# Kernel optimization log

Measured on AMD Instinct MI355X. Metric: run time of the kernel, lower is better.

## Reference

```python
import jax, jax.numpy as jnp
import numpy as np

DIM = 512
NUM_GROUPS = 32
EPS = 1e-6
INV_SQRT2 = 0.7071067811865476


def group_norm(x, gamma, beta):
    # x: [b, c, h, w]; GroupNorm with NUM_GROUPS groups, per-channel affine
    b, c, h, w = x.shape
    xg = x.reshape(b, NUM_GROUPS, c // NUM_GROUPS, h, w)
    mu = xg.mean(axis=(2, 3, 4), keepdims=True)
    var = xg.var(axis=(2, 3, 4), keepdims=True)
    xn = ((xg - mu) * jax.lax.rsqrt(var + EPS)).reshape(b, c, h, w)
    return xn * gamma[None, :, None, None] + beta[None, :, None, None]


def conv1x1(x, w, b):
    # 1x1 conv == per-pixel GEMM over channels. w: [out_c, in_c], b: [out_c]
    return jnp.einsum('oc,bchw->bohw', w, x) + b[None, :, None, None]


def setup_inputs() -> dict:
    key = jax.random.key(0)
    ks = jax.random.split(key, 6)
    b, c, h, w = 4, DIM, 64, 64
    q = jax.random.normal(ks[0], (b, c, h, w), dtype=jnp.float32)
    init = lambda k: jax.random.normal(k, (DIM, DIM), dtype=jnp.float32) * 0.02
    return {
        'q': q,
        'gamma': jnp.ones((DIM,), jnp.float32),
        'beta': jnp.zeros((DIM,), jnp.float32),
        'wq': init(ks[1]), 'bq': jnp.zeros((DIM,), jnp.float32),
        'wk': init(ks[2]), 'bk': jnp.zeros((DIM,), jnp.float32),
        'wv': init(ks[3]), 'bv': jnp.zeros((DIM,), jnp.float32),
        'wo': init(ks[4]), 'bo': jnp.zeros((DIM,), jnp.float32),
    }


def reference(q, gamma, beta, wq, bq, wk, bk, wv, bv, wo, bo):
    q_in = q
    x = group_norm(q, gamma, beta)  # self-attention path: v is None -> v = normed q
    qp = conv1x1(x, wq, bq)
    kp = conv1x1(x, wk, bk)
    vp = conv1x1(x, wv, bv)
    b, c, h, w = qp.shape
    qf = qp.reshape(b, c, h * w)
    kf = kp.reshape(b, c, h * w)
    vf = vp.reshape(b, c, h * w)
    # scores[b, i, j] = sum_c k[b,c,i] * q[b,c,j]; softmax over i (key axis, dim=-2)
    scores = jnp.einsum('bci,bcj->bij', kf, qf) * (c ** -0.5)
    attn = jax.nn.softmax(scores, axis=-2)
    out = jnp.einsum('bci,bij->bcj', vf, attn).reshape(b, c, h, w)
    out = conv1x1(out, wo, bo)
    return (out + q_in) * INV_SQRT2
```

## Files before the change

### kernel.cpp

```cpp
#include <hip/hip_runtime.h>

typedef __bf16 bf16;
typedef __bf16 bf16x4 __attribute__((ext_vector_type(4)));
typedef __bf16 bf16x8 __attribute__((ext_vector_type(8)));
typedef float floatx4 __attribute__((ext_vector_type(4)));
typedef float floatx16 __attribute__((ext_vector_type(16)));

#define SCALE_QK 0.044194173824159216f
#define INV_SQRT2F 0.7071067811865476f
#define TEN  8388608L
#define SBAT 2097152L

typedef const __attribute__((address_space(1))) void GV;
typedef __attribute__((address_space(3))) void SV;

__global__ __launch_bounds__(256) void detect_k(
    const unsigned* __restrict__ q, int* __restrict__ flag)
{
    __shared__ int cnt;
    if (threadIdx.x == 0) cnt = 0;
    __syncthreads();
    int c = 0;
    for (int i = threadIdx.x; i < 4096; i += 256) {
        unsigned e = (q[i] >> 7) & 0xFFu;
        c += (e >= 100u && e <= 140u) ? 1 : 0;
    }
    atomicAdd(&cnt, c);
    __syncthreads();
    if (threadIdx.x == 0) *flag = (cnt < 3000) ? 1 : 0;
}

__global__ __launch_bounds__(256) void convw_k(
    const void* w0, const void* w1, const void* w2, const void* w3,
    bf16* __restrict__ dst, const int* __restrict__ flag)
{
    const void* srcs[4] = {w0, w1, w2, w3};
    const void* s = srcs[blockIdx.y];
    bf16* d = dst + (size_t)blockIdx.y * 262144;
    const int i = (blockIdx.x * 256 + threadIdx.x) * 8;
    bf16x8 v;
    if (*flag) {
        const float* f = (const float*)s;
        #pragma unroll
        for (int r = 0; r < 8; ++r) v[r] = (bf16)f[i + r];
    } else {
        v = *(const bf16x8*)((const bf16*)s + i);
    }
    *(bf16x8*)(d + i) = v;
}

__global__ __launch_bounds__(256) void convp_k(
    const void* p0, const void* p1, const void* p2,
    const void* p3, const void* p4, const void* p5,
    float* __restrict__ dst, const int* __restrict__ flag)
{
    const void* srcs[6] = {p0, p1, p2, p3, p4, p5};
    const int f = *flag;
    for (int i = threadIdx.x; i < 3072; i += 256) {
        const void* s = srcs[i >> 9];
        const int off = i & 511;
        dst[i] = f ? ((const float*)s)[off] : (float)((const bf16*)s)[off];
    }
}

__global__ __launch_bounds__(256) void groupnorm_k(
    const void* __restrict__ qraw, const float* __restrict__ gamma,
    const float* __restrict__ beta, bf16* __restrict__ XN,
    const int* __restrict__ flag)
{
    const int tid = threadIdx.x;
    const int b = blockIdx.x >> 5, g = blockIdx.x & 31;
    const int f32 = *flag;
    const size_t base = ((size_t)b * 512 + (size_t)g * 16) * 4096;
    const float* sf = (const float*)qraw + base;
    const bf16*  sb = (const bf16*)qraw + base;

    float sum = 0.f, sq = 0.f;
    if (f32) {
        const floatx4* v4 = (const floatx4*)sf;
        for (int idx = tid; idx < 16384; idx += 256) {
            floatx4 v = v4[idx];
            #pragma unroll
            for (int r = 0; r < 4; ++r) { float f = v[r]; sum += f; sq += f * f; }
        }
    } else {
        const bf16x8* v8 = (const bf16x8*)sb;
        for (int idx = tid; idx < 8192; idx += 256) {
            bf16x8 v = v8[idx];
            #pragma unroll
            for (int r = 0; r < 8; ++r) { float f = (float)v[r]; sum += f; sq += f * f; }
        }
    }
    #pragma unroll
    for (int off = 32; off; off >>= 1) {
        sum += __shfl_down(sum, off);
        sq  += __shfl_down(sq, off);
    }
    __shared__ float sS[4], sQ[4];
    __shared__ float s_mean, s_rstd;
    const int wave = tid >> 6, lane = tid & 63;
    if (lane == 0) { sS[wave] = sum; sQ[wave] = sq; }
    __syncthreads();
    if (tid == 0) {
        float ts = sS[0] + sS[1] + sS[2] + sS[3];
        float tq = sQ[0] + sQ[1] + sQ[2] + sQ[3];
        float mean = ts * (1.0f / 65536.0f);
        float var  = tq * (1.0f / 65536.0f) - mean * mean;
        s_mean = mean;
        s_rstd = rsqrtf(fmaxf(var, 0.f) + 1e-6f);
    }
    __syncthreads();
    const float mean = s_mean, rstd = s_rstd;

    float ga[16], be[16];
    #pragma unroll
    for (int c = 0; c < 16; ++c) {
        ga[c] = gamma[g * 16 + c] * rstd;
        be[c] = beta[g * 16 + c] - mean * ga[c];
    }
    bf16* dst = XN + (size_t)b * SBAT + (size_t)g * 16;
    for (int p0 = 0; p0 < 4096; p0 += 256) {
        const int p = p0 + tid;
        bf16x8 o0, o1;
        #pragma unroll
        for (int c = 0; c < 8; ++c) {
            float v = f32 ? sf[(size_t)c * 4096 + p] : (float)sb[(size_t)c * 4096 + p];
            o0[c] = (bf16)(v * ga[c] + be[c]);
        }
        #pragma unroll
        for (int c = 0; c < 8; ++c) {
            float v = f32 ? sf[(size_t)(c + 8) * 4096 + p] : (float)sb[(size_t)(c + 8) * 4096 + p];
            o1[c] = (bf16)(v * ga[c + 8] + be[c + 8]);
        }
        bf16* dp = dst + (size_t)p * 512;
        *(bf16x8*)dp = o0;
        *(bf16x8*)(dp + 8) = o1;
    }
}

__global__ __launch_bounds__(512, 1) void fused_attn(
    const bf16* __restrict__ QKt,
    const bf16* __restrict__ V,
    bf16* __restrict__ AOt)
{
    __shared__ __align__(16) char smc[147456];

    const int tid = threadIdx.x;
    const int w = tid >> 6, lane = tid & 63;
    const int fr = lane & 15, quad = lane >> 4;
    const int l5 = lane >> 5, l31 = lane & 31;

    const int ll = blockIdx.x;
    const int xcd = ll & 7, rr = ll >> 3;
    const int b = xcd >> 1;
    const int j0 = ((xcd & 1) * 32 + rr) * 64;

    const bf16* Qb = QKt + (size_t)b * 4194304;
    const bf16* Kb = Qb + 512;
    const bf16* Vb = V + (size_t)b * SBAT;

    const int jb = w >> 1;
    const int kb = w & 1;
    const int wmP = (w >> 2) * 32;
    const int wnP = (w & 3) * 128;

    bf16x8 qf[16];
    {
        const bf16* qsrc = Qb + (size_t)(j0 + jb * 16 + fr) * 1024 + quad * 8;
        #pragma unroll
        for (int s = 0; s < 16; ++s) qf[s] = *(const bf16x8*)(qsrc + s * 32);
    }

    const int lcK = ((tid & 15) ^ ((tid >> 4) & 7)) << 3;
    const int rowK = tid >> 4;
    auto stageK = [&](int key0, int kd0, int buf) {
        char* d = smc + buf * 32768;
        const bf16* s0 = Kb + (size_t)(key0 + rowK) * 1024 + kd0 + lcK;
        #pragma unroll
        for (int rho = 0; rho < 4; ++rho)
            __builtin_amdgcn_global_load_lds((GV*)(s0 + (size_t)rho * 32 * 1024),
                (SV*)(d + rho * 8192 + tid * 16), 16, 0, 0);
    };
    const int lcV = ((tid & 3) ^ ((tid >> 3) & 3)) << 3;
    const int rowV = tid >> 2;
    auto stageV = [&](int i0, int buf) {
        char* d = smc + 65536 + buf * 32768;
        const bf16* s0 = Vb + (size_t)rowV * 4096 + i0 + lcV;
        #pragma unroll
        for (int rho = 0; rho < 4; ++rho)
            __builtin_amdgcn_global_load_lds((GV*)(s0 + (size_t)rho * 128 * 4096),
                (SV*)(d + rho * 8192 + tid * 16), 16, 0, 0);
    };

    const int kxor = fr & 7;
    const int kaddr0 = (kb * 64 + fr) * 256;
    const int prow_ = jb * 16 + fr;
    const int pxor = (prow_ & 7) << 4;
    char* const pbase = smc + 131072 + prow_ * 256;

    const int prowR = wmP + l31;
    const int swzP = (prowR & 7) << 4;

    floatx16 acc_o[4] = {};
    float l_acc = 0.f;

    stageK(0, 0, 0);

    for (int c = 0; c < 32; ++c) {
        const int k0 = c * 128;
        floatx4 acc_s[4] = {};

        #pragma unroll
        for (int s = 0; s < 4; ++s) {
            asm volatile("s_waitcnt vmcnt(0)" ::: "memory");
            __builtin_amdgcn_s_barrier();
            if (s < 3) stageK(k0, (s + 1) * 128, (s + 1) & 1);
            else       stageV(k0, 0);
            const char* kbuf = smc + (s & 1) * 32768;
            __builtin_amdgcn_s_setprio(1);
            #pragma unroll
            for (int ksl = 0; ksl < 4; ++ksl) {
                #pragma unroll
                for (int kf = 0; kf < 4; ++kf) {
                    bf16x8 kf8 = *(const bf16x8*)(kbuf + kaddr0 + kf * 4096 +
                        ((((ksl << 2) | quad) ^ kxor) << 4));
                    acc_s[kf] = __builtin_amdgcn_mfma_f32_16x16x32_bf16(
                        kf8, qf[s * 4 + ksl], acc_s[kf], 0, 0, 0);
                }
            }
            __builtin_amdgcn_s_setprio(0);
        }

        {
            float rs = 0.f;
            #pragma unroll
            for (int kf = 0; kf < 4; ++kf) {
                bf16x4 pk;
                #pragma unroll
                for (int r = 0; r < 4; ++r) {
                    float e = __expf(fminf(acc_s[kf][r] * SCALE_QK, 30.f));
                    rs += e;
                    pk[r] = (bf16)e;
                }
                *(bf16x4*)(pbase + ((kb * 128 + kf * 32 + quad * 8) ^ pxor)) = pk;
            }
            rs += __shfl_xor(rs, 16);
            rs += __shfl_xor(rs, 32);
            l_acc += rs;
            asm volatile("s_waitcnt lgkmcnt(0)" ::: "memory");
        }

        #pragma unroll
        for (int sv = 0; sv < 4; ++sv) {
            asm volatile("s_waitcnt vmcnt(0)" ::: "memory");
            __builtin_amdgcn_s_barrier();
            if (sv < 3)          stageV(k0 + (sv + 1) * 32, (sv + 1) & 1);
            else if (c < 31)     stageK(k0 + 128, 0, 0);
            const char* vb = smc + 65536 + (sv & 1) * 32768;
            const char* pb = smc + 131072;
            __builtin_amdgcn_s_setprio(1);
            #pragma unroll
            for (int ih = 0; ih < 2; ++ih) {
                const int is = sv * 2 + ih;
                bf16x8 pa = *(const bf16x8*)(pb + prowR * 256 +
                    ((is * 32 + l5 * 16) ^ swzP));
                #pragma unroll
                for (int nf = 0; nf < 4; ++nf) {
                    const int cc = wnP + nf * 32 + l31;
                    bf16x8 vb8 = *(const bf16x8*)(vb + cc * 64 +
                        ((ih * 32 + l5 * 16) ^ (((cc >> 1) & 3) << 4)));
                    acc_o[nf] = __builtin_amdgcn_mfma_f32_32x32x16_bf16(
                        pa, vb8, acc_o[nf], 0, 0, 0);
                }
            }
            __builtin_amdgcn_s_setprio(0);
        }
    }
    asm volatile("s_waitcnt vmcnt(0)" ::: "memory");
    __syncthreads();

    float* lsh = (float*)smc;
    if (lane < 16) lsh[w * 16 + lane] = l_acc;
    __syncthreads();
    float* rsh = (float*)(smc + 512);
    if (tid < 64) {
        const int jbq = tid >> 4, t = tid & 15;
        rsh[tid] = 1.0f / fmaxf(lsh[jbq * 32 + t] + lsh[jbq * 32 + 16 + t], 1e-30f);
    }
    __syncthreads();

    bf16* out = AOt + (size_t)b * SBAT + (size_t)j0 * 512;
    #pragma unroll
    for (int reg = 0; reg < 16; ++reg) {
        const int j = wmP + (reg & 3) + 8 * (reg >> 2) + 4 * l5;
        const float rl = rsh[j];
        #pragma unroll
        for (int nf = 0; nf < 4; ++nf) {
            const int cc = wnP + nf * 32 + l31;
            out[(size_t)j * 512 + cc] = (bf16)(acc_o[nf][reg] * rl);
        }
    }
}

template <int EPI>
__global__ __launch_bounds__(256, 4) void gemm_xyt(
    const bf16* __restrict__ Xb, const bf16* __restrict__ Yb,
    void* __restrict__ Cv, int N, int K, int lda, int ldb,
    long sX, long sY, long sC,
    const float* __restrict__ bias,
    const void* __restrict__ res, long sR,
    const int* __restrict__ flag)
{
    __shared__ __align__(16) bf16 smem[17408];

    const int tid  = threadIdx.x;
    const int wave = tid >> 6;
    const int lane = tid & 63;
    const int z = blockIdx.z;

    int bx = blockIdx.x, by = blockIdx.y;
    {
        const int gx = gridDim.x, gy = gridDim.y;
        const int o = by * gx + bx;
        const int xcd = o & 7, idx = o >> 3;
        if (gx == 8) {
            bx = xcd;
            by = idx;
        } else if (gx == 32 && gy == 4) {
            bx = (xcd & 1) * 16 + (idx & 15);
            by = xcd >> 1;
        }
    }

    const bf16* X = Xb + (long)z * sX;
    const bf16* Y = Yb + (long)z * sY;
    bf16*  Cb = (bf16*)Cv  + (long)z * sC;
    float* Cf = (float*)Cv + (long)z * sC;
    const int f32o = (EPI == 4) ? *flag : 0;

    const int m0 = by * 128, n0 = bx * 128;
    const int wm = (wave >> 1) * 64, wn = (wave & 1) * 64;
    const int fr = lane & 15, quad = lane >> 4;

    const int srow = tid >> 2;
    const int scol = (tid & 3) * 8;
    const bf16* pX = X + (size_t)(m0 + srow) * lda + scol;
    const bf16* pY = Y + (size_t)(n0 + srow) * ldb + scol;
    const size_t oX = (size_t)64 * lda, oY = (size_t)64 * ldb;
    char* const sb0 = (char*)smem;
    const int ldst = tid * 16;

    auto stage = [&](int k, int pb) {
        char* d = sb0 + pb * 16384;
        const bf16* x = pX + k * 32;
        const bf16* y = pY + k * 32;
        __builtin_amdgcn_global_load_lds((GV*)x,        (SV*)(d + ldst),         16, 0, 0);
        __builtin_amdgcn_global_load_lds((GV*)(x + oX), (SV*)(d + 4096 + ldst),  16, 0, 0);
        __builtin_amdgcn_global_load_lds((GV*)y,        (SV*)(d + 8192 + ldst),  16, 0, 0);
        __builtin_amdgcn_global_load_lds((GV*)(y + oY), (SV*)(d + 12288 + ldst), 16, 0, 0);
    };

    floatx4 acc[4][4] = {};
    const int NK = K >> 5;

    stage(0, 0);
    __syncthreads();

    for (int k = 0; k < NK; ++k) {
        const int p = k & 1;
        if (k + 1 < NK) stage(k + 1, 1 - p);
        const bf16* bA = smem + p * 8192;
        const bf16* bB = bA + 4096;
        bf16x8 af[4], bfr[4];
        #pragma unroll
        for (int i = 0; i < 4; ++i) {
            af[i]  = *(const bf16x8*)&bA[(wm + i * 16 + fr) * 32 + quad * 8];
            bfr[i] = *(const bf16x8*)&bB[(wn + i * 16 + fr) * 32 + quad * 8];
        }
        #pragma unroll
        for (int i = 0; i < 4; ++i)
            #pragma unroll
            for (int j = 0; j < 4; ++j)
                acc[i][j] = __builtin_amdgcn_mfma_f32_16x16x32_bf16(
                    af[i], bfr[j], acc[i][j], 0, 0, 0);
        __syncthreads();
    }

    #pragma unroll
    for (int i = 0; i < 4; ++i) {
        const int mg = m0 + wm + i * 16 + quad * 4;
        float bmr[4];
        if (EPI == 1 || EPI == 4) {
            #pragma unroll
            for (int r = 0; r < 4; ++r) bmr[r] = bias[mg + r];
        }
        #pragma unroll
        for (int j = 0; j < 4; ++j) {
            const int ng = n0 + wn + j * 16 + fr;
            #pragma unroll
            for (int r = 0; r < 4; ++r) {
                float v = acc[i][j][r];
                if (EPI == 0) v += bias[ng];
                if (EPI == 1) v += bmr[r];
                if (EPI == 4) v += bmr[r];
                acc[i][j][r] = v;
            }
        }
    }

    if (EPI != 4) {
        bf16* ct = smem;
        #pragma unroll
        for (int i = 0; i < 4; ++i)
            #pragma unroll
            for (int j = 0; j < 4; ++j)
                #pragma unroll
                for (int r = 0; r < 4; ++r)
                    ct[(wm + i * 16 + quad * 4 + r) * 132 + wn + j * 16 + fr] =
                        (bf16)acc[i][j][r];
        __syncthreads();
        #pragma unroll
        for (int w = 0; w < 8; ++w) {
            const int idx = w * 2048 + tid * 8;
            const int row = idx >> 7, col = idx & 127;
            bf16x8 v = *(const bf16x8*)&ct[row * 132 + col];
            *(bf16x8*)&Cb[(size_t)(m0 + row) * N + n0 + col] = v;
        }
    } else if (f32o) {
        float* ct = (float*)smem;
        const float* rres = (const float*)res + (size_t)z * sR;
        #pragma unroll
        for (int h = 0; h < 2; ++h) {
            if ((wave >> 1) == h) {
                #pragma unroll
                for (int i = 0; i < 4; ++i)
                    #pragma unroll
                    for (int j = 0; j < 4; ++j)
                        #pragma unroll
                        for (int r = 0; r < 4; ++r)
                            ct[(i * 16 + quad * 4 + r) * 132 + wn + j * 16 + fr] =
                                acc[i][j][r];
            }
            __syncthreads();
            #pragma unroll
            for (int w = 0; w < 8; ++w) {
                const int idx = (w * 256 + tid) * 4;
                const int row = idx >> 7, col = idx & 127;
                const size_t o = (size_t)(m0 + h * 64 + row) * N + n0 + col;
                floatx4 v = *(const floatx4*)&ct[row * 132 + col];
                floatx4 rv = *(const floatx4*)&rres[o];
                #pragma unroll
                for (int e = 0; e < 4; ++e) v[e] = (v[e] + rv[e]) * INV_SQRT2F;
                *(floatx4*)&Cf[o] = v;
            }
            __syncthreads();
        }
    } else {
        const bf16* resb = (const bf16*)res + (size_t)z * sR;
        #pragma unroll
        for (int i = 0; i < 4; ++i) {
            const int mg = m0 + wm + i * 16 + quad * 4;
            #pragma unroll
            for (int j = 0; j < 4; ++j) {
                const int ng = n0 + wn + j * 16 + fr;
                #pragma unroll
                for (int r = 0; r < 4; ++r) {
                    const size_t o = (size_t)(mg + r) * N + ng;
                    Cb[o] = (bf16)((acc[i][j][r] + (float)resb[o]) * INV_SQRT2F);
                }
            }
        }
    }
}

extern "C" void kernel_launch(void* const* d_in, const int* in_sizes, int n_in,
                              void* d_out, int out_size, void* d_ws, size_t ws_size,
                              hipStream_t stream)
{
    const void* q     = d_in[0];
    const void* gamma = d_in[1];
    const void* beta  = d_in[2];
    const void* wq    = d_in[3];
    const void* bq    = d_in[4];
    const void* wk    = d_in[5];
    const void* bk    = d_in[6];
    const void* wv    = d_in[7];
    const void* bv    = d_in[8];
    const void* wo    = d_in[9];
    const void* bo    = d_in[10];

    char* w = (char*)d_ws;
    int*   flag = (int*)w;   w += 16;
    float* Pf   = (float*)w; w += 6 * 512 * 4;
    bf16*  Wc   = (bf16*)w;  w += 4 * 262144 * 2;
    bf16*  XN   = (bf16*)w;  w += TEN * 2;
    bf16*  QKt  = (bf16*)w;  w += (size_t)4 * 4096 * 1024 * 2;
    bf16*  V    = (bf16*)w;  w += TEN * 2;
    bf16*  AOt  = XN;

    detect_k<<<dim3(1), 256, 0, stream>>>((const unsigned*)q, flag);
    convw_k<<<dim3(128, 4), 256, 0, stream>>>(wq, wk, wv, wo, Wc, flag);
    convp_k<<<dim3(1), 256, 0, stream>>>(gamma, beta, bq, bk, bv, bo, Pf, flag);

    groupnorm_k<<<dim3(128), 256, 0, stream>>>(q, Pf, Pf + 512, XN, flag);

    gemm_xyt<0><<<dim3(8, 32, 4), 256, 0, stream>>>(XN, Wc, QKt,
        1024, 512, 512, 512, SBAT, 0, (long)4096 * 1024, Pf + 1024,
        nullptr, 0, flag);
    gemm_xyt<1><<<dim3(32, 4, 4), 256, 0, stream>>>(Wc + 2 * 262144, XN, V,
        4096, 512, 512, 512, 0, SBAT, SBAT, Pf + 2048,
        nullptr, 0, flag);

    fused_attn<<<dim3(256), 512, 0, stream>>>(QKt, V, AOt);

    gemm_xyt<4><<<dim3(32, 4, 4), 256, 0, stream>>>(Wc + 3 * 262144, AOt, d_out,
        4096, 512, 512, 512, 0, SBAT, SBAT, Pf + 2560,
        q, SBAT, flag);
}
```

Measured before the change: 473.4 us.

## Warp-specialize attention kernel: QK/softmax waves and PV waves run software-pipelined

Splits the 8 waves of the attention block into two roles. Four waves compute QK^T scores and the exp for each 128-key chunk, while the other four compute the P·V accumulation for the previous chunk. Each stage now issues both the K and V loads, so the QK and PV phases of consecutive chunks overlap instead of running back to back. The cost is per-wave register pressure (8 score accumulators, or 2x4 32x32 accumulators), one extra pipeline iteration, and added barriers. The K swizzle widens to 16 rows, and the P buffer is now single-buffered while being shared across chunks.

```diff
diff --git a/kernel.cpp b/kernel.cpp
--- a/kernel.cpp
+++ b/kernel.cpp
@@ -159,19 +159,7 @@
     const bf16* Kb = Qb + 512;
     const bf16* Vb = V + (size_t)b * SBAT;
 
-    const int jb = w >> 1;
-    const int kb = w & 1;
-    const int wmP = (w >> 2) * 32;
-    const int wnP = (w & 3) * 128;
-
-    bf16x8 qf[16];
-    {
-        const bf16* qsrc = Qb + (size_t)(j0 + jb * 16 + fr) * 1024 + quad * 8;
-        #pragma unroll
-        for (int s = 0; s < 16; ++s) qf[s] = *(const bf16x8*)(qsrc + s * 32);
-    }
-
-    const int lcK = ((tid & 15) ^ ((tid >> 4) & 7)) << 3;
+    const int lcK = ((tid & 15) ^ ((tid >> 4) & 15)) << 3;
     const int rowK = tid >> 4;
     auto stageK = [&](int key0, int kd0, int buf) {
         char* d = smc + buf * 32768;
@@ -191,113 +179,139 @@
             __builtin_amdgcn_global_load_lds((GV*)(s0 + (size_t)rho * 128 * 4096),
                 (SV*)(d + rho * 8192 + tid * 16), 16, 0, 0);
     };
-
-    const int kxor = fr & 7;
-    const int kaddr0 = (kb * 64 + fr) * 256;
-    const int prow_ = jb * 16 + fr;
-    const int pxor = (prow_ & 7) << 4;
-    char* const pbase = smc + 131072 + prow_ * 256;
-
-    const int prowR = wmP + l31;
-    const int swzP = (prowR & 7) << 4;
-
-    floatx16 acc_o[4] = {};
-    float l_acc = 0.f;
-
-    stageK(0, 0, 0);
-
-    for (int c = 0; c < 32; ++c) {
-        const int k0 = c * 128;
-        floatx4 acc_s[4] = {};
-
-        #pragma unroll
-        for (int s = 0; s < 4; ++s) {
-            asm volatile("s_waitcnt vmcnt(0)" ::: "memory");
+    auto stage_sub = [&](int cc, int s) {
+        if (s < 3) {
+            if (cc < 32) stageK(cc * 128, (s + 1) * 128, (s + 1) & 1);
+            if (cc >= 1 && cc <= 32)
+                stageV((cc - 1) * 128 + (s + 1) * 32, (s + 1) & 1);
+        } else {
+            if (cc < 31) stageK((cc + 1) * 128, 0, 0);
+            if (cc < 32) stageV(cc * 128, 0);
+        }
+    };
+
+    float* lsh = (float*)(smc + 131072 + 16384);
+
+    if (w < 4) {
+        const int jb = w;
+        bf16x8 qf[16];
+        {
+            const bf16* qsrc = Qb + (size_t)(j0 + jb * 16 + fr) * 1024 + quad * 8;
+            #pragma unroll
+            for (int s = 0; s < 16; ++s) qf[s] = *(const bf16x8*)(qsrc + s * 32);
+        }
+        const int prow = jb * 16 + fr;
+        const int pxor = (prow & 15) << 4;
+        char* const pbase = smc + 131072 + prow * 256;
+        float l_acc = 0.f;
+
+        stageK(0, 0, 0);
+
+        for (int cc = 0; cc <= 32; ++cc) {
+            floatx4 acc_s[8] = {};
+            #pragma unroll
+            for (int s = 0; s < 4; ++s) {
+                asm volatile("s_waitcnt vmcnt(0)" ::: "memory");
+                __builtin_amdgcn_s_barrier();
+                stage_sub(cc, s);
+                if (cc < 32) {
+                    const char* kbuf = smc + (s & 1) * 32768;
+                    __builtin_amdgcn_s_setprio(1);
+                    #pragma unroll
+                    for (int ksl = 0; ksl < 4; ++ksl) {
+                        const char* kb0 = kbuf + fr * 256 +
+                            ((((ksl << 2) | quad) ^ fr) << 4);
+                        #pragma unroll
+                        for (int kf = 0; kf < 8; ++kf) {
+                            bf16x8 kf8 = *(const bf16x8*)(kb0 + kf * 4096);
+                            acc_s[kf] = __builtin_amdgcn_mfma_f32_16x16x32_bf16(
+                                kf8, qf[s * 4 + ksl], acc_s[kf], 0, 0, 0);
+                        }
+                    }
+                    __builtin_amdgcn_s_setprio(0);
+                }
+            }
             __builtin_amdgcn_s_barrier();
-            if (s < 3) stageK(k0, (s + 1) * 128, (s + 1) & 1);
-            else       stageV(k0, 0);
-            const char* kbuf = smc + (s & 1) * 32768;
-            __builtin_amdgcn_s_setprio(1);
-            #pragma unroll
-            for (int ksl = 0; ksl < 4; ++ksl) {
+            if (cc < 32) {
+                float rs = 0.f;
                 #pragma unroll
-                for (int kf = 0; kf < 4; ++kf) {
-                    bf16x8 kf8 = *(const bf16x8*)(kbuf + kaddr0 + kf * 4096 +
-                        ((((ksl << 2) | quad) ^ kxor) << 4));
-                    acc_s[kf] = __builtin_amdgcn_mfma_f32_16x16x32_bf16(
-                        kf8, qf[s * 4 + ksl], acc_s[kf], 0, 0, 0);
+                for (int kf = 0; kf < 8; ++kf) {
+                    bf16x4 pk;
+                    #pragma unroll
+                    for (int r = 0; r < 4; ++r) {
+                        float e = __expf(fminf(acc_s[kf][r] * SCALE_QK, 30.f));
+                        rs += e;
+                        pk[r] = (bf16)e;
+                    }
+                    *(bf16x4*)(pbase + ((kf * 32 + quad * 8) ^ pxor)) = pk;
                 }
-            }
-            __builtin_amdgcn_s_setprio(0);
-        }
-
-        {
-            float rs = 0.f;
-            #pragma unroll
-            for (int kf = 0; kf < 4; ++kf) {
-                bf16x4 pk;
-                #pragma unroll
-                for (int r = 0; r < 4; ++r) {
-                    float e = __expf(fminf(acc_s[kf][r] * SCALE_QK, 30.f));
-                    rs += e;
-                    pk[r] = (bf16)e;
+                rs += __shfl_xor(rs, 16);
+                rs += __shfl_xor(rs, 32);
+                l_acc += rs;
+                asm volatile("s_waitcnt lgkmcnt(0)" ::: "memory");
+            }
+            __builtin_amdgcn_s_barrier();
+        }
+        float* lout = (float*)smc;
+        if (lane < 16) lout[jb * 16 + lane] = l_acc;
+        __syncthreads();
+    } else {
+        const int pw = w - 4;
+        floatx16 acc_o[2][4] = {};
+
+
+        for (int cc = 0; cc <= 32; ++cc) {
+            #pragma unroll
+            for (int s = 0; s < 4; ++s) {
+                asm volatile("s_waitcnt vmcnt(0)" ::: "memory");
+                __builtin_amdgcn_s_barrier();
+                stage_sub(cc, s);
+                if (cc >= 1) {
+                    const char* vb = smc + 65536 + (s & 1) * 32768;
+                    const char* pb = smc + 131072;
+                    __builtin_amdgcn_s_setprio(1);
+                    #pragma unroll
+                    for (int t = 0; t < 2; ++t) {
+                        bf16x8 pa[2];
+                        #pragma unroll
+                        for (int jf = 0; jf < 2; ++jf) {
+                            const int pr = jf * 32 + l31;
+                            pa[jf] = *(const bf16x8*)(pb + pr * 256 +
+                                (((s * 2 + t) * 32 + l5 * 16) ^ ((pr & 15) << 4)));
+                        }
+                        #pragma unroll
+                        for (int nf = 0; nf < 4; ++nf) {
+                            const int vc = pw * 128 + nf * 32 + l31;
+                            bf16x8 vb8 = *(const bf16x8*)(vb + vc * 64 +
+                                ((t * 32 + l5 * 16) ^ (((vc >> 1) & 3) << 4)));
+                            acc_o[0][nf] = __builtin_amdgcn_mfma_f32_32x32x16_bf16(
+                                pa[0], vb8, acc_o[0][nf], 0, 0, 0);
+                            acc_o[1][nf] = __builtin_amdgcn_mfma_f32_32x32x16_bf16(
+                                pa[1], vb8, acc_o[1][nf], 0, 0, 0);
+                        }
+                    }
+                    __builtin_amdgcn_s_setprio(0);
                 }
-                *(bf16x4*)(pbase + ((kb * 128 + kf * 32 + quad * 8) ^ pxor)) = pk;
-            }
-            rs += __shfl_xor(rs, 16);
-            rs += __shfl_xor(rs, 32);
-            l_acc += rs;
-            asm volatile("s_waitcnt lgkmcnt(0)" ::: "memory");
-        }
-
-        #pragma unroll
-        for (int sv = 0; sv < 4; ++sv) {
-            asm volatile("s_waitcnt vmcnt(0)" ::: "memory");
+            }
             __builtin_amdgcn_s_barrier();
-            if (sv < 3)          stageV(k0 + (sv + 1) * 32, (sv + 1) & 1);
-            else if (c < 31)     stageK(k0 + 128, 0, 0);
-            const char* vb = smc + 65536 + (sv & 1) * 32768;
-            const char* pb = smc + 131072;
-            __builtin_amdgcn_s_setprio(1);
-            #pragma unroll
-            for (int ih = 0; ih < 2; ++ih) {
-                const int is = sv * 2 + ih;
-                bf16x8 pa = *(const bf16x8*)(pb + prowR * 256 +
-                    ((is * 32 + l5 * 16) ^ swzP));
+            __builtin_amdgcn_s_barrier();
+        }
+        __syncthreads();
+        const float* lout = (const float*)smc;
+
+        bf16* out = AOt + (size_t)b * SBAT + (size_t)j0 * 512;
+        #pragma unroll
+        for (int jf = 0; jf < 2; ++jf) {
+            #pragma unroll
+            for (int reg = 0; reg < 16; ++reg) {
+                const int j = jf * 32 + (reg & 3) + 8 * (reg >> 2) + 4 * l5;
+                const float rl = 1.0f / fmaxf(lout[j], 1e-30f);
                 #pragma unroll
                 for (int nf = 0; nf < 4; ++nf) {
-                    const int cc = wnP + nf * 32 + l31;
-                    bf16x8 vb8 = *(const bf16x8*)(vb + cc * 64 +
-                        ((ih * 32 + l5 * 16) ^ (((cc >> 1) & 3) << 4)));
-                    acc_o[nf] = __builtin_amdgcn_mfma_f32_32x32x16_bf16(
-                        pa, vb8, acc_o[nf], 0, 0, 0);
+                    const int d = pw * 128 + nf * 32 + l31;
+                    out[(size_t)j * 512 + d] = (bf16)(acc_o[jf][nf][reg] * rl);
                 }
             }
-            __builtin_amdgcn_s_setprio(0);
-        }
-    }
-    asm volatile("s_waitcnt vmcnt(0)" ::: "memory");
-    __syncthreads();
-
-    float* lsh = (float*)smc;
-    if (lane < 16) lsh[w * 16 + lane] = l_acc;
-    __syncthreads();
-    float* rsh = (float*)(smc + 512);
-    if (tid < 64) {
-        const int jbq = tid >> 4, t = tid & 15;
-        rsh[tid] = 1.0f / fmaxf(lsh[jbq * 32 + t] + lsh[jbq * 32 + 16 + t], 1e-30f);
-    }
-    __syncthreads();
-
-    bf16* out = AOt + (size_t)b * SBAT + (size_t)j0 * 512;
-    #pragma unroll
-    for (int reg = 0; reg < 16; ++reg) {
-        const int j = wmP + (reg & 3) + 8 * (reg >> 2) + 4 * l5;
-        const float rl = rsh[j];
-        #pragma unroll
-        for (int nf = 0; nf < 4; ++nf) {
-            const int cc = wnP + nf * 32 + l31;
-            out[(size_t)j * 512 + cc] = (bf16)(acc_o[nf][reg] * rl);
         }
     }
 }
```

After: 453.0 us. 1.04x faster.
